# Performance work log

Hardware: AMD Instinct MI355X
Metric: run time of the kernel (lower is better)

The kernel has to match this reference:

```python
import jax, jax.numpy as jnp
import numpy as np

B, C, H, W = 64, 64, 64, 64  # C = num_features (time + C-1 space dims)
EPS = 1e-5  # module eps; also used as numerical clamp like the torch manifold


def setup_inputs() -> dict:
    key = jax.random.key(0)
    k1, k2 = jax.random.split(key)
    # Valid Lorentz (k=1) points: x0 = sqrt(1 + ||x_space||^2)
    xs = 0.5 * jax.random.normal(k1, (B, C - 1, H, W), dtype=jnp.float32)
    x0 = jnp.sqrt(1.0 + jnp.sum(xs * xs, axis=1, keepdims=True))
    x = jnp.concatenate([x0, xs], axis=1)  # [B, C, H, W]
    gamma = 0.5 + jax.random.uniform(k2, (C - 1,), dtype=jnp.float32)
    beta = 0.05 * jax.random.normal(jax.random.fold_in(key, 7), (C - 1,), dtype=jnp.float32)
    return {"x": x, "gamma": gamma, "beta": beta}


def reference(x, gamma, beta):
    Bn, Cn, Hn, Wn = x.shape
    xf = x.transpose(0, 2, 3, 1).reshape(-1, Cn)  # [N, C], N = B*H*W

    # Lorentz midpoint (centroid): mean, then normalize by Lorentz norm
    m = jnp.mean(xf, axis=0)                      # [C]
    mm = m[0] * m[0] - jnp.sum(m[1:] * m[1:])     # -<m,m>_L (positive for timelike)
    mu = m / jnp.sqrt(jnp.maximum(mm, EPS))       # [C], on hyperboloid

    # alpha = -<x, mu>_L  (>= 1 on the manifold)
    alpha = xf[:, 0] * mu[0] - xf[:, 1:] @ mu[1:]          # [N]
    alpha = jnp.maximum(alpha, 1.0 + EPS)

    # geodesic distance & Frechet variance
    d = jnp.arccosh(alpha)                                  # [N]
    var = jnp.mean(d * d)

    # logmap at mu: v = d/sqrt(alpha^2-1) * (x - alpha*mu)
    coef = d / jnp.sqrt(alpha * alpha - 1.0)
    v = coef[:, None] * (xf - alpha[:, None] * mu[None, :])  # [N, C]

    # parallel transport mu -> origin o=(1,0,...):
    # PT(v) = v + <o,v>_L/(1 - <mu,o>_L) * (mu + o) = v - v0/(1+mu0) * (mu + o)
    mu_plus_o = mu.at[0].add(1.0)
    vo = v - (v[:, 0] / (1.0 + mu[0]))[:, None] * mu_plus_o[None, :]

    # scale/shift space components, then orthogonal projection back to manifold
    vs = vo[:, 1:]                                           # [N, C-1]
    s = gamma[None, :] * vs / (jnp.sqrt(var) + EPS) + beta[None, :]
    t = jnp.sqrt(1.0 + jnp.sum(s * s, axis=1, keepdims=True))
    out = jnp.concatenate([t, s], axis=1)                    # [N, C]

    return out.reshape(Bn, Hn, Wn, Cn).transpose(0, 3, 1, 2)
```

## Files before the change

kernel.cpp:

```cpp
#include <hip/hip_runtime.h>
#include <math.h>

#define BDIM 64
#define CDIM 64
#define HWN  4096
#define NROWS (BDIM * HWN)
#define CHSTRIDE (CDIM * HWN)
#define EPSV 1e-5f

#define ROWBLOCKS (NROWS / 256)

#define DD_OFF    4096
#define ALPHA_OFF 8192
#define COEF_OFF  (ALPHA_OFF + NROWS)

__global__ __launch_bounds__(256) void k_chansum(const float* __restrict__ x,
                                                 float* __restrict__ ws) {
    const int plane = blockIdx.x;
    const float4* p4 = reinterpret_cast<const float4*>(x + (size_t)plane * HWN);
    float s = 0.f;
#pragma unroll
    for (int i = 0; i < HWN / 4 / 256; ++i) {
        float4 v = p4[threadIdx.x + i * 256];
        s += (v.x + v.y) + (v.z + v.w);
    }
    for (int off = 32; off; off >>= 1) s += __shfl_down(s, off, 64);
    __shared__ float red[4];
    const int lane = threadIdx.x & 63, wid = threadIdx.x >> 6;
    if (lane == 0) red[wid] = s;
    __syncthreads();
    if (threadIdx.x == 0) ws[plane] = (red[0] + red[1]) + (red[2] + red[3]);
}

__device__ __forceinline__ void compute_mu(const float* __restrict__ ws,
                                           float* smu, float* stmp) {
    const int t = threadIdx.x, c = t & 63, g = t >> 6;
    float m = 0.f;
#pragma unroll
    for (int b = 0; b < BDIM / 4; ++b) m += ws[(g * (BDIM / 4) + b) * CDIM + c];
    stmp[g * 64 + c] = m;
    __syncthreads();
    if (t < 64) {
        const float msum = (stmp[c] + stmp[64 + c]) + (stmp[128 + c] + stmp[192 + c]);
        const float mval = msum * (1.0f / (float)NROWS);
        float mm = (c == 0) ? mval * mval : -mval * mval;
        for (int off = 32; off; off >>= 1) mm += __shfl_down(mm, off, 64);
        mm = __shfl(mm, 0, 64);
        smu[c] = mval / sqrtf(fmaxf(mm, EPSV));
    }
    __syncthreads();
}

__global__ __launch_bounds__(256) void k_alpha(const float* __restrict__ x,
                                               float* __restrict__ ws) {
    __shared__ float smu[64];
    __shared__ float stmp[256];
    compute_mu(ws, smu, stmp);

    const int n = blockIdx.x * 256 + threadIdx.x;
    const int b = n >> 12;
    const int hw = n & (HWN - 1);
    const float* p = x + (size_t)b * CHSTRIDE + hw;

    float alpha = p[0] * smu[0];
#pragma unroll
    for (int c = 1; c < CDIM; ++c) alpha -= p[(size_t)c * HWN] * smu[c];
    alpha = fmaxf(alpha, 1.0f + EPSV);
    const float d = acoshf(alpha);
    const float coef = d / sqrtf(alpha * alpha - 1.0f);
    ws[ALPHA_OFF + n] = alpha;
    ws[COEF_OFF + n]  = coef;

    float dd = d * d;
    for (int off = 32; off; off >>= 1) dd += __shfl_down(dd, off, 64);
    __shared__ float red[4];
    const int lane = threadIdx.x & 63, wid = threadIdx.x >> 6;
    if (lane == 0) red[wid] = dd;
    __syncthreads();
    if (threadIdx.x == 0)
        ws[DD_OFF + blockIdx.x] = (red[0] + red[1]) + (red[2] + red[3]);
}

__global__ __launch_bounds__(256) void k_out(const float* __restrict__ x,
                                             const float* __restrict__ gamma,
                                             const float* __restrict__ beta,
                                             float* __restrict__ out,
                                             const float* __restrict__ ws) {
    __shared__ float smu[64], sg[64], sb[64];
    __shared__ float stmp[256];
    compute_mu(ws, smu, stmp);

    float pd = ws[DD_OFF + threadIdx.x] + ws[DD_OFF + 256 + threadIdx.x] +
               ws[DD_OFF + 512 + threadIdx.x] + ws[DD_OFF + 768 + threadIdx.x];
    for (int off = 32; off; off >>= 1) pd += __shfl_down(pd, off, 64);
    const int lane = threadIdx.x & 63, wid = threadIdx.x >> 6;
    if (lane == 0) stmp[wid] = pd;
    if (threadIdx.x < 64) {
        sg[threadIdx.x] = (threadIdx.x >= 1) ? gamma[threadIdx.x - 1] : 0.f;
        sb[threadIdx.x] = (threadIdx.x >= 1) ? beta[threadIdx.x - 1] : 0.f;
    }
    __syncthreads();
    const float varsum = (stmp[0] + stmp[1]) + (stmp[2] + stmp[3]);
    const float var = varsum * (1.0f / (float)NROWS);
    const float inv_sv = 1.0f / (sqrtf(var) + EPSV);

    const int n = blockIdx.x * 256 + threadIdx.x;
    const int b = n >> 12;
    const int hw = n & (HWN - 1);
    const size_t base = (size_t)b * CHSTRIDE + hw;
    const float* p = x + base;
    float* op = out + base;

    const float al = ws[ALPHA_OFF + n];
    const float co = ws[COEF_OFF + n];
    const float m0 = smu[0];
    const float kk = co * (p[0] - al * m0) / (1.0f + m0);

    float s2 = 0.f;
#pragma unroll
    for (int c = 1; c < CDIM; ++c) {
        const float xv = p[(size_t)c * HWN];
        const float m = smu[c];
        const float v = co * (xv - al * m);
        const float vo = v - kk * m;
        const float s = sg[c] * vo * inv_sv + sb[c];
        s2 += s * s;
        op[(size_t)c * HWN] = s;
    }
    op[0] = sqrtf(1.0f + s2);
}

extern "C" void kernel_launch(void* const* d_in, const int* in_sizes, int n_in,
                              void* d_out, int out_size, void* d_ws, size_t ws_size,
                              hipStream_t stream) {
    const float* x     = (const float*)d_in[0];
    const float* gamma = (const float*)d_in[1];
    const float* beta  = (const float*)d_in[2];
    float* out = (float*)d_out;
    float* ws  = (float*)d_ws;

    k_chansum<<<BDIM * CDIM, 256, 0, stream>>>(x, ws);
    k_alpha<<<ROWBLOCKS, 256, 0, stream>>>(x, ws);
    k_out<<<ROWBLOCKS, 256, 0, stream>>>(x, gamma, beta, out, ws);
}
```

Baseline: 137.8 us.

## Stage channel tiles in LDS with float4 loads/stores in alpha and output kernels

```diff
diff --git a/kernel.cpp b/kernel.cpp
--- a/kernel.cpp
+++ b/kernel.cpp
@@ -8,7 +8,8 @@
 #define CHSTRIDE (CDIM * HWN)
 #define EPSV 1e-5f
 
-#define ROWBLOCKS (NROWS / 256)
+#define TILE 256
+#define ROWBLOCKS (NROWS / TILE)
 
 #define DD_OFF    4096
 #define ALPHA_OFF 8192
@@ -51,34 +52,53 @@
     __syncthreads();
 }
 
+__device__ __forceinline__ void load_tile(const float* __restrict__ base,
+                                          float* __restrict__ tile) {
+    const int w = threadIdx.x >> 6, l = threadIdx.x & 63;
+#pragma unroll
+    for (int s = 0; s < 16; ++s) {
+        const int c = s * 4 + w;
+        const float4 v = *reinterpret_cast<const float4*>(base + (size_t)c * HWN + 4 * l);
+        *reinterpret_cast<float4*>(&tile[c * TILE + 4 * l]) = v;
+    }
+}
+
 __global__ __launch_bounds__(256) void k_alpha(const float* __restrict__ x,
                                                float* __restrict__ ws) {
-    __shared__ float smu[64];
-    __shared__ float stmp[256];
-    compute_mu(ws, smu, stmp);
+    __shared__ float tile[CDIM * TILE];
+    __shared__ float smu[64], red[4];
+    compute_mu(ws, smu, tile);
 
-    const int n = blockIdx.x * 256 + threadIdx.x;
-    const int b = n >> 12;
-    const int hw = n & (HWN - 1);
-    const float* p = x + (size_t)b * CHSTRIDE + hw;
+    const int n0 = blockIdx.x * TILE;
+    const int b = n0 >> 12;
+    const int hw0 = n0 & (HWN - 1);
+    load_tile(x + (size_t)b * CHSTRIDE + hw0, tile);
+    __syncthreads();
 
-    float alpha = p[0] * smu[0];
+    const int t = threadIdx.x;
+    float a0 = tile[t] * smu[0]           - tile[TILE + t] * smu[1];
+    float a1 = -tile[2 * TILE + t] * smu[2] - tile[3 * TILE + t] * smu[3];
+    float a2 = 0.f, a3 = 0.f;
 #pragma unroll
-    for (int c = 1; c < CDIM; ++c) alpha -= p[(size_t)c * HWN] * smu[c];
+    for (int c = 4; c < CDIM; c += 4) {
+        a0 -= tile[(c + 0) * TILE + t] * smu[c + 0];
+        a1 -= tile[(c + 1) * TILE + t] * smu[c + 1];
+        a2 -= tile[(c + 2) * TILE + t] * smu[c + 2];
+        a3 -= tile[(c + 3) * TILE + t] * smu[c + 3];
+    }
+    float alpha = (a0 + a1) + (a2 + a3);
     alpha = fmaxf(alpha, 1.0f + EPSV);
     const float d = acoshf(alpha);
     const float coef = d / sqrtf(alpha * alpha - 1.0f);
-    ws[ALPHA_OFF + n] = alpha;
-    ws[COEF_OFF + n]  = coef;
+    ws[ALPHA_OFF + n0 + t] = alpha;
+    ws[COEF_OFF + n0 + t]  = coef;
 
     float dd = d * d;
     for (int off = 32; off; off >>= 1) dd += __shfl_down(dd, off, 64);
-    __shared__ float red[4];
-    const int lane = threadIdx.x & 63, wid = threadIdx.x >> 6;
+    const int lane = t & 63, wid = t >> 6;
     if (lane == 0) red[wid] = dd;
     __syncthreads();
-    if (threadIdx.x == 0)
-        ws[DD_OFF + blockIdx.x] = (red[0] + red[1]) + (red[2] + red[3]);
+    if (t == 0) ws[DD_OFF + blockIdx.x] = (red[0] + red[1]) + (red[2] + red[3]);
 }
 
 __global__ __launch_bounds__(256) void k_out(const float* __restrict__ x,
@@ -86,48 +106,60 @@
                                              const float* __restrict__ beta,
                                              float* __restrict__ out,
                                              const float* __restrict__ ws) {
-    __shared__ float smu[64], sg[64], sb[64];
-    __shared__ float stmp[256];
-    compute_mu(ws, smu, stmp);
+    __shared__ float tile[CDIM * TILE];
+    __shared__ float smu[64], sg[64], sb[64], svar[4];
+    compute_mu(ws, smu, tile);
 
-    float pd = ws[DD_OFF + threadIdx.x] + ws[DD_OFF + 256 + threadIdx.x] +
-               ws[DD_OFF + 512 + threadIdx.x] + ws[DD_OFF + 768 + threadIdx.x];
-    for (int off = 32; off; off >>= 1) pd += __shfl_down(pd, off, 64);
-    const int lane = threadIdx.x & 63, wid = threadIdx.x >> 6;
-    if (lane == 0) stmp[wid] = pd;
-    if (threadIdx.x < 64) {
-        sg[threadIdx.x] = (threadIdx.x >= 1) ? gamma[threadIdx.x - 1] : 0.f;
-        sb[threadIdx.x] = (threadIdx.x >= 1) ? beta[threadIdx.x - 1] : 0.f;
+    {
+        float pd = ws[DD_OFF + threadIdx.x] + ws[DD_OFF + 256 + threadIdx.x] +
+                   ws[DD_OFF + 512 + threadIdx.x] + ws[DD_OFF + 768 + threadIdx.x];
+        for (int off = 32; off; off >>= 1) pd += __shfl_down(pd, off, 64);
+        const int lane = threadIdx.x & 63, wid = threadIdx.x >> 6;
+        if (lane == 0) svar[wid] = pd;
+        if (threadIdx.x < 64) {
+            sg[threadIdx.x] = (threadIdx.x >= 1) ? gamma[threadIdx.x - 1] : 0.f;
+            sb[threadIdx.x] = (threadIdx.x >= 1) ? beta[threadIdx.x - 1] : 0.f;
+        }
     }
     __syncthreads();
-    const float varsum = (stmp[0] + stmp[1]) + (stmp[2] + stmp[3]);
-    const float var = varsum * (1.0f / (float)NROWS);
+    const float var = ((svar[0] + svar[1]) + (svar[2] + svar[3])) * (1.0f / (float)NROWS);
     const float inv_sv = 1.0f / (sqrtf(var) + EPSV);
 
-    const int n = blockIdx.x * 256 + threadIdx.x;
-    const int b = n >> 12;
-    const int hw = n & (HWN - 1);
-    const size_t base = (size_t)b * CHSTRIDE + hw;
-    const float* p = x + base;
-    float* op = out + base;
+    const int n0 = blockIdx.x * TILE;
+    const int b = n0 >> 12;
+    const int hw0 = n0 & (HWN - 1);
+    const size_t gbase = (size_t)b * CHSTRIDE + hw0;
+    load_tile(x + gbase, tile);
+    __syncthreads();
 
-    const float al = ws[ALPHA_OFF + n];
-    const float co = ws[COEF_OFF + n];
+    const int t = threadIdx.x;
+    const float al = ws[ALPHA_OFF + n0 + t];
+    const float co = ws[COEF_OFF + n0 + t];
     const float m0 = smu[0];
-    const float kk = co * (p[0] - al * m0) / (1.0f + m0);
+    const float kk = co * (tile[t] - al * m0) / (1.0f + m0);
 
     float s2 = 0.f;
 #pragma unroll
     for (int c = 1; c < CDIM; ++c) {
-        const float xv = p[(size_t)c * HWN];
+        const float xv = tile[c * TILE + t];
         const float m = smu[c];
         const float v = co * (xv - al * m);
         const float vo = v - kk * m;
-        const float s = sg[c] * vo * inv_sv + sb[c];
+        const float s = (sg[c] * inv_sv) * vo + sb[c];
         s2 += s * s;
-        op[(size_t)c * HWN] = s;
+        tile[c * TILE + t] = s;
     }
-    op[0] = sqrtf(1.0f + s2);
+    tile[t] = sqrtf(1.0f + s2);
+    __syncthreads();
+
+    const int w = t >> 6, l = t & 63;
+    float* obase = out + gbase;
+#pragma unroll
+    for (int s = 0; s < 16; ++s) {
+        const int c = s * 4 + w;
+        const float4 v = *reinterpret_cast<const float4*>(&tile[c * TILE + 4 * l]);
+        *reinterpret_cast<float4*>(obase + (size_t)c * HWN + 4 * l) = v;
+    }
 }
 
 extern "C" void kernel_launch(void* const* d_in, const int* in_sizes, int n_in,
```

New measurement: 142.5 us. +3.4%, slower.
